# Performance work log

Measured on AMD Instinct MI355X. Metric: run time of the kernel, lower is better.

The kernel has to match this reference:

```python
import jax, jax.numpy as jnp
import numpy as np

B = 8192
D_IN = 1024
H = 1024
N_LAYERS = 10  # 1 input layer + 9 hidden layers, then output layer H->1


def setup_inputs() -> dict:
    key = jax.random.key(0)
    ks = jax.random.split(key, 7)
    s_in = 1.0 / np.sqrt(D_IN)
    s_h = 1.0 / np.sqrt(H)
    return {
        "x": jax.random.normal(ks[0], (B, D_IN), dtype=jnp.float32),
        "W0": jax.random.normal(ks[1], (H, D_IN), dtype=jnp.float32) * s_in,
        "b0": jax.random.normal(ks[2], (H,), dtype=jnp.float32) * s_in,
        "Wh": jax.random.normal(ks[3], (N_LAYERS - 1, H, H), dtype=jnp.float32) * s_h,
        "bh": jax.random.normal(ks[4], (N_LAYERS - 1, H), dtype=jnp.float32) * s_h,
        "Wout": jax.random.normal(ks[5], (1, H), dtype=jnp.float32) * s_h,
        "bout": jax.random.normal(ks[6], (1,), dtype=jnp.float32) * s_h,
    }


def reference(x, W0, b0, Wh, bh, Wout, bout):
    # First layer: Linear(D_IN -> H) + sigmoid. torch Linear is x @ W.T + b.
    h = jax.nn.sigmoid(x @ W0.T + b0)  # [B, H]

    # Remaining num_layers-1 hidden layers, identical shape -> lax.scan over stacked weights.
    def step(h, wb):
        W, b = wb
        return jax.nn.sigmoid(h @ W.T + b), None

    h, _ = jax.lax.scan(step, h, (Wh, bh))

    # Output layer: Linear(H -> 1), no activation.
    return h @ Wout.T + bout  # [B, 1]
```

## Files before the change

### kernel.cpp

```cpp
#include <hip/hip_runtime.h>
#include <stdint.h>

typedef unsigned short u16;
typedef unsigned int   u32;
typedef _Float16 f16;
typedef __attribute__((ext_vector_type(4))) float    f32x4;
typedef __attribute__((ext_vector_type(8))) _Float16 f16x8;
typedef __attribute__((ext_vector_type(4))) _Float16 f16x4;

#define DIM    1024
#define NROWS  8192
#define NLAYER 10

__device__ __forceinline__ void gl_lds16(const void* g, void* l) {
    __builtin_amdgcn_global_load_lds((const __attribute__((address_space(1))) u32*)g,
                                     (__attribute__((address_space(3))) u32*)l, 16, 0, 0);
}

__global__ __launch_bounds__(256) void conv_weights(const float* __restrict__ W0,
                                                    const float* __restrict__ Wh,
                                                    f16* __restrict__ Wf) {
    int i = (blockIdx.x * 256 + threadIdx.x) * 4;
    const float* src = (i < 1048576) ? (W0 + i) : (Wh + (i - 1048576));
    float4 w = *(const float4*)src;
    f16x4 o;
    o.x = (f16)w.x; o.y = (f16)w.y; o.z = (f16)w.z; o.w = (f16)w.w;
    *(f16x4*)(Wf + i) = o;
}

__global__ __launch_bounds__(256) void conv_x(const float* __restrict__ x,
                                              f16* __restrict__ Af) {
    int i = (blockIdx.x * 256 + threadIdx.x) * 4;
    float4 w = *(const float4*)(x + i);
    f16x4 o;
    o.x = (f16)w.x; o.y = (f16)w.y; o.z = (f16)w.z; o.w = (f16)w.w;
    *(f16x4*)(Af + i) = o;
}

#define ABUF_B 0
#define BBUF_B 16384
#define BUFSZ  32768
#define NKT    16

__global__ __launch_bounds__(256, 2) void layer_gemm(
        const f16* __restrict__ A,
        const f16* __restrict__ Bg,
        const float* __restrict__ bias,
        f16* __restrict__ O) {
    __shared__ char lds[2 * BUFSZ];

    int bid = blockIdx.x;
    int swz = (bid & 7) * 64 + (bid >> 3);
    int bn = swz & 7;
    int bm = swz >> 3;

    const int tid  = threadIdx.x;
    const int lane = tid & 63;
    const int wid  = tid >> 6;
    const int wr   = wid >> 1;
    const int wc   = wid & 1;

    const int swcol = (((lane & 7) ^ ((lane >> 3) & 7)) << 4);
    const char* gsrc[8];
    u32 ldst[8];
    #pragma unroll
    for (int j = 0; j < 8; ++j) {
        int c = wid * 8 + j;
        if (c < 16) {
            int grow = bm * 128 + c * 8 + (lane >> 3);
            gsrc[j] = (const char*)A + (size_t)grow * 2048 + swcol;
            ldst[j] = ABUF_B + c * 1024;
        } else {
            int c2 = c - 16;
            int grow = bn * 128 + c2 * 8 + (lane >> 3);
            gsrc[j] = (const char*)Bg + (size_t)grow * 2048 + swcol;
            ldst[j] = BBUF_B + c2 * 1024;
        }
    }

    f32x4 acc[4][4];
    #pragma unroll
    for (int mf = 0; mf < 4; ++mf)
        #pragma unroll
        for (int nf = 0; nf < 4; ++nf)
            acc[mf][nf] = (f32x4){0.f, 0.f, 0.f, 0.f};

    #pragma unroll
    for (int j = 0; j < 8; ++j)
        gl_lds16(gsrc[j], lds + ldst[j]);
    __syncthreads();

    for (int kt = 0; kt < NKT; ++kt) {
        const char* base = lds + (kt & 1) * BUFSZ;
        if (kt < NKT - 1) {
            char* nb = lds + ((kt + 1) & 1) * BUFSZ;
            #pragma unroll
            for (int j = 0; j < 8; ++j)
                gl_lds16(gsrc[j] + (size_t)(kt + 1) * 128, nb + ldst[j]);
        }

        #pragma unroll
        for (int ks = 0; ks < 2; ++ks) {
            f16x8 a[4], b[4];
            const int cb = ks * 64 + ((lane >> 4) << 4);
            #pragma unroll
            for (int mf = 0; mf < 4; ++mf) {
                int r = wr * 64 + mf * 16 + (lane & 15);
                int byt = r * 128 + (cb ^ ((r & 7) << 4));
                a[mf] = *(const f16x8*)(base + ABUF_B + byt);
            }
            #pragma unroll
            for (int nf = 0; nf < 4; ++nf) {
                int r = wc * 64 + nf * 16 + (lane & 15);
                int byt = r * 128 + (cb ^ ((r & 7) << 4));
                b[nf] = *(const f16x8*)(base + BBUF_B + byt);
            }
            __builtin_amdgcn_s_setprio(1);
            #pragma unroll
            for (int mf = 0; mf < 4; ++mf)
                #pragma unroll
                for (int nf = 0; nf < 4; ++nf)
                    acc[mf][nf] = __builtin_amdgcn_mfma_f32_16x16x32_f16(b[nf], a[mf], acc[mf][nf], 0, 0, 0);
            __builtin_amdgcn_s_setprio(0);
        }
        __syncthreads();
    }

    #pragma unroll
    for (int nf = 0; nf < 4; ++nf) {
        int gn0 = bn * 128 + wc * 64 + nf * 16 + ((lane >> 4) << 2);
        f32x4 b4 = *(const f32x4*)(bias + gn0);
        #pragma unroll
        for (int mf = 0; mf < 4; ++mf) {
            int gm = bm * 128 + wr * 64 + mf * 16 + (lane & 15);
            f16x4 o;
            #pragma unroll
            for (int j = 0; j < 4; ++j) {
                float z = acc[mf][nf][j] + b4[j];
                o[j] = (f16)(1.0f / (1.0f + __expf(-z)));
            }
            *(f16x4*)(O + (size_t)gm * DIM + gn0) = o;
        }
    }
}

__global__ __launch_bounds__(256) void out_gemv(const f16* __restrict__ A,
                                                const float* __restrict__ Wout,
                                                const float* __restrict__ bout,
                                                float* __restrict__ out) {
    int wid  = threadIdx.x >> 6;
    int lane = threadIdx.x & 63;
    int row  = blockIdx.x * 4 + wid;
    const f16* p = A + (size_t)row * DIM + lane * 16;
    const float* pw = Wout + lane * 16;
    float s = 0.f;
    #pragma unroll
    for (int i = 0; i < 4; ++i) {
        f16x4 h4 = *(const f16x4*)(p + i * 4);
        float4 w4 = *(const float4*)(pw + i * 4);
        s += (float)h4.x * w4.x + (float)h4.y * w4.y + (float)h4.z * w4.z + (float)h4.w * w4.w;
    }
    #pragma unroll
    for (int off = 32; off > 0; off >>= 1)
        s += __shfl_down(s, off);
    if (lane == 0) out[row] = s + bout[0];
}

extern "C" void kernel_launch(void* const* d_in, const int* in_sizes, int n_in,
                              void* d_out, int out_size, void* d_ws, size_t ws_size,
                              hipStream_t stream) {
    const float* x    = (const float*)d_in[0];
    const float* W0   = (const float*)d_in[1];
    const float* b0   = (const float*)d_in[2];
    const float* Wh   = (const float*)d_in[3];
    const float* bh   = (const float*)d_in[4];
    const float* Wout = (const float*)d_in[5];
    const float* bout = (const float*)d_in[6];
    float* out = (float*)d_out;

    f16* ws = (f16*)d_ws;
    f16* Wf = ws;
    f16* A0 = Wf + (size_t)NLAYER * DIM * DIM;
    f16* A1 = A0 + (size_t)NROWS * DIM;

    conv_weights<<<NLAYER * DIM * DIM / 1024, 256, 0, stream>>>(W0, Wh, Wf);
    conv_x<<<NROWS * DIM / 1024, 256, 0, stream>>>(x, A0);

    const f16* in = A0;
    f16* o = A1;
    for (int l = 0; l < NLAYER; ++l) {
        const float* bias = (l == 0) ? b0 : (bh + (size_t)(l - 1) * DIM);
        layer_gemm<<<512, 256, 0, stream>>>(in, Wf + (size_t)l * DIM * DIM, bias, o);
        f16* t = (f16*)in; in = o; o = t;
    }

    out_gemv<<<NROWS / 4, 256, 0, stream>>>(in, Wout, bout, out);
}
```

Baseline: 269.0 us.

## Prepack weights into MFMA fragment layout and load B directly to registers

Weights are converted into a fragment-packed layout so each lane can load its MFMA B operand straight from global memory into registers, bypassing LDS. The GEMM tile grows to 256x128 with 512 threads, and only the A tile is staged through double-buffered LDS, which cuts LDS traffic and reuses each B fragment across more rows. The cost is B loads going directly from global/L2 with latency exposed inside the k-loop, plus only 256 blocks on the device.

```diff
diff --git a/kernel.cpp b/kernel.cpp
--- a/kernel.cpp
+++ b/kernel.cpp
@@ -17,15 +17,26 @@
                                      (__attribute__((address_space(3))) u32*)l, 16, 0, 0);
 }
 
+__device__ __forceinline__ f16 cvt16(float x) { return (f16)x; }
+
 __global__ __launch_bounds__(256) void conv_weights(const float* __restrict__ W0,
                                                     const float* __restrict__ Wh,
-                                                    f16* __restrict__ Wf) {
-    int i = (blockIdx.x * 256 + threadIdx.x) * 4;
-    const float* src = (i < 1048576) ? (W0 + i) : (Wh + (i - 1048576));
-    float4 w = *(const float4*)src;
-    f16x4 o;
-    o.x = (f16)w.x; o.y = (f16)w.y; o.z = (f16)w.z; o.w = (f16)w.w;
-    *(f16x4*)(Wf + i) = o;
+                                                    f16* __restrict__ Wp) {
+    int g    = blockIdx.x * 4 + (threadIdx.x >> 6);
+    int lane = threadIdx.x & 63;
+    int lz   = g >> 11;
+    int rem  = g & 2047;
+    int n16  = rem >> 5;
+    int kc   = rem & 31;
+    int n  = n16 * 16 + (lane & 15);
+    int k0 = kc * 32 + (lane >> 4) * 8;
+    const float* src = (lz == 0 ? W0 : Wh + (size_t)(lz - 1) * DIM * DIM) + (size_t)n * DIM + k0;
+    float4 w0 = *(const float4*)src;
+    float4 w1 = *(const float4*)(src + 4);
+    f16x8 o;
+    o[0]=cvt16(w0.x); o[1]=cvt16(w0.y); o[2]=cvt16(w0.z); o[3]=cvt16(w0.w);
+    o[4]=cvt16(w1.x); o[5]=cvt16(w1.y); o[6]=cvt16(w1.z); o[7]=cvt16(w1.w);
+    *(f16x8*)((char*)Wp + (size_t)g * 1024 + lane * 16) = o;
 }
 
 __global__ __launch_bounds__(256) void conv_x(const float* __restrict__ x,
@@ -37,20 +48,18 @@
     *(f16x4*)(Af + i) = o;
 }
 
-#define ABUF_B 0
-#define BBUF_B 16384
-#define BUFSZ  32768
-#define NKT    16
-
-__global__ __launch_bounds__(256, 2) void layer_gemm(
+#define ABUF  32768
+#define NKT   16
+
+__global__ __launch_bounds__(512, 2) void layer_gemm(
         const f16* __restrict__ A,
-        const f16* __restrict__ Bg,
+        const f16* __restrict__ Bp,
         const float* __restrict__ bias,
         f16* __restrict__ O) {
-    __shared__ char lds[2 * BUFSZ];
+    __shared__ char lds[2 * ABUF];
 
     int bid = blockIdx.x;
-    int swz = (bid & 7) * 64 + (bid >> 3);
+    int swz = (bid & 7) * 32 + (bid >> 3);
     int bn = swz & 7;
     int bm = swz >> 3;
 
@@ -61,22 +70,18 @@
     const int wc   = wid & 1;
 
     const int swcol = (((lane & 7) ^ ((lane >> 3) & 7)) << 4);
-    const char* gsrc[8];
-    u32 ldst[8];
-    #pragma unroll
-    for (int j = 0; j < 8; ++j) {
-        int c = wid * 8 + j;
-        if (c < 16) {
-            int grow = bm * 128 + c * 8 + (lane >> 3);
-            gsrc[j] = (const char*)A + (size_t)grow * 2048 + swcol;
-            ldst[j] = ABUF_B + c * 1024;
-        } else {
-            int c2 = c - 16;
-            int grow = bn * 128 + c2 * 8 + (lane >> 3);
-            gsrc[j] = (const char*)Bg + (size_t)grow * 2048 + swcol;
-            ldst[j] = BBUF_B + c2 * 1024;
-        }
-    }
+    const char* gsrc[4];
+    u32 ldst[4];
+    #pragma unroll
+    for (int j = 0; j < 4; ++j) {
+        int c = wid * 4 + j;
+        int grow = bm * 256 + c * 8 + (lane >> 3);
+        gsrc[j] = (const char*)A + (size_t)grow * 2048 + swcol;
+        ldst[j] = c * 1024;
+    }
+
+    const char* bptr = (const char*)Bp
+                     + ((size_t)(bn * 8 + wc * 4) * 32) * 1024 + lane * 16;
 
     f32x4 acc[4][4];
     #pragma unroll
@@ -86,41 +91,42 @@
             acc[mf][nf] = (f32x4){0.f, 0.f, 0.f, 0.f};
 
     #pragma unroll
-    for (int j = 0; j < 8; ++j)
+    for (int j = 0; j < 4; ++j)
         gl_lds16(gsrc[j], lds + ldst[j]);
     __syncthreads();
 
     for (int kt = 0; kt < NKT; ++kt) {
-        const char* base = lds + (kt & 1) * BUFSZ;
+        f16x8 b[2][4];
+        #pragma unroll
+        for (int ks = 0; ks < 2; ++ks)
+            #pragma unroll
+            for (int nf = 0; nf < 4; ++nf)
+                b[ks][nf] = *(const f16x8*)(bptr + ((size_t)(nf * 32 + kt * 2 + ks)) * 1024);
+
         if (kt < NKT - 1) {
-            char* nb = lds + ((kt + 1) & 1) * BUFSZ;
-            #pragma unroll
-            for (int j = 0; j < 8; ++j)
+            char* nb = lds + ((kt + 1) & 1) * ABUF;
+            #pragma unroll
+            for (int j = 0; j < 4; ++j)
                 gl_lds16(gsrc[j] + (size_t)(kt + 1) * 128, nb + ldst[j]);
         }
 
+        const char* base = lds + (kt & 1) * ABUF;
         #pragma unroll
         for (int ks = 0; ks < 2; ++ks) {
-            f16x8 a[4], b[4];
+            f16x8 a[4];
             const int cb = ks * 64 + ((lane >> 4) << 4);
             #pragma unroll
             for (int mf = 0; mf < 4; ++mf) {
                 int r = wr * 64 + mf * 16 + (lane & 15);
                 int byt = r * 128 + (cb ^ ((r & 7) << 4));
-                a[mf] = *(const f16x8*)(base + ABUF_B + byt);
-            }
-            #pragma unroll
-            for (int nf = 0; nf < 4; ++nf) {
-                int r = wc * 64 + nf * 16 + (lane & 15);
-                int byt = r * 128 + (cb ^ ((r & 7) << 4));
-                b[nf] = *(const f16x8*)(base + BBUF_B + byt);
+                a[mf] = *(const f16x8*)(base + byt);
             }
             __builtin_amdgcn_s_setprio(1);
             #pragma unroll
             for (int mf = 0; mf < 4; ++mf)
                 #pragma unroll
                 for (int nf = 0; nf < 4; ++nf)
-                    acc[mf][nf] = __builtin_amdgcn_mfma_f32_16x16x32_f16(b[nf], a[mf], acc[mf][nf], 0, 0, 0);
+                    acc[mf][nf] = __builtin_amdgcn_mfma_f32_16x16x32_f16(b[ks][nf], a[mf], acc[mf][nf], 0, 0, 0);
             __builtin_amdgcn_s_setprio(0);
         }
         __syncthreads();
@@ -132,7 +138,7 @@
         f32x4 b4 = *(const f32x4*)(bias + gn0);
         #pragma unroll
         for (int mf = 0; mf < 4; ++mf) {
-            int gm = bm * 128 + wr * 64 + mf * 16 + (lane & 15);
+            int gm = bm * 256 + wr * 64 + mf * 16 + (lane & 15);
             f16x4 o;
             #pragma unroll
             for (int j = 0; j < 4; ++j) {
@@ -179,18 +185,18 @@
     float* out = (float*)d_out;
 
     f16* ws = (f16*)d_ws;
-    f16* Wf = ws;
-    f16* A0 = Wf + (size_t)NLAYER * DIM * DIM;
+    f16* Wp = ws;
+    f16* A0 = Wp + (size_t)NLAYER * DIM * DIM;
     f16* A1 = A0 + (size_t)NROWS * DIM;
 
-    conv_weights<<<NLAYER * DIM * DIM / 1024, 256, 0, stream>>>(W0, Wh, Wf);
+    conv_weights<<<NLAYER * 2048 / 4, 256, 0, stream>>>(W0, Wh, Wp);
     conv_x<<<NROWS * DIM / 1024, 256, 0, stream>>>(x, A0);
 
     const f16* in = A0;
     f16* o = A1;
     for (int l = 0; l < NLAYER; ++l) {
         const float* bias = (l == 0) ? b0 : (bh + (size_t)(l - 1) * DIM);
-        layer_gemm<<<512, 256, 0, stream>>>(in, Wf + (size_t)l * DIM * DIM, bias, o);
+        layer_gemm<<<256, 512, 0, stream>>>(in, Wp + (size_t)l * DIM * DIM, bias, o);
         f16* t = (f16*)in; in = o; o = t;
     }
 
```

Result: slower. 316.8 us (+17.8%).

## Single-buffer LDS in layer GEMM for higher occupancy and fuse conversion kernels

Applied to the files above, without the earlier changes.

Removes the double-buffered LDS prefetch in the layer GEMM, using one 32KB tile buffer loaded then synchronized each k-step, and raises the launch-bounds occupancy hint to 4 blocks per CU. Also merges the weight and input fp32->fp16 conversion kernels into a single launch. The intent is to rely on more resident blocks rather than software prefetch for latency hiding, but the grid of 512 blocks may not fill the extra slots, exposing load latency and tightening register limits.

```diff
diff --git a/kernel.cpp b/kernel.cpp
--- a/kernel.cpp
+++ b/kernel.cpp
@@ -17,37 +17,40 @@
                                      (__attribute__((address_space(3))) u32*)l, 16, 0, 0);
 }
 
-__global__ __launch_bounds__(256) void conv_weights(const float* __restrict__ W0,
-                                                    const float* __restrict__ Wh,
-                                                    f16* __restrict__ Wf) {
-    int i = (blockIdx.x * 256 + threadIdx.x) * 4;
-    const float* src = (i < 1048576) ? (W0 + i) : (Wh + (i - 1048576));
+#define WELEMS (NLAYER * DIM * DIM)
+#define XELEMS (NROWS * DIM)
+__global__ __launch_bounds__(256) void conv_all(const float* __restrict__ x,
+                                                const float* __restrict__ W0,
+                                                const float* __restrict__ Wh,
+                                                f16* __restrict__ Wf,
+                                                f16* __restrict__ A0) {
+    size_t i = ((size_t)blockIdx.x * 256 + threadIdx.x) * 4;
+    const float* src;
+    f16* dst;
+    if (i < WELEMS) {
+        src = (i < DIM * DIM) ? (W0 + i) : (Wh + (i - DIM * DIM));
+        dst = Wf + i;
+    } else {
+        size_t k = i - WELEMS;
+        src = x + k;
+        dst = A0 + k;
+    }
     float4 w = *(const float4*)src;
     f16x4 o;
     o.x = (f16)w.x; o.y = (f16)w.y; o.z = (f16)w.z; o.w = (f16)w.w;
-    *(f16x4*)(Wf + i) = o;
-}
-
-__global__ __launch_bounds__(256) void conv_x(const float* __restrict__ x,
-                                              f16* __restrict__ Af) {
-    int i = (blockIdx.x * 256 + threadIdx.x) * 4;
-    float4 w = *(const float4*)(x + i);
-    f16x4 o;
-    o.x = (f16)w.x; o.y = (f16)w.y; o.z = (f16)w.z; o.w = (f16)w.w;
-    *(f16x4*)(Af + i) = o;
+    *(f16x4*)dst = o;
 }
 
 #define ABUF_B 0
 #define BBUF_B 16384
-#define BUFSZ  32768
 #define NKT    16
 
-__global__ __launch_bounds__(256, 2) void layer_gemm(
+__global__ __launch_bounds__(256, 4) void layer_gemm(
         const f16* __restrict__ A,
         const f16* __restrict__ Bg,
         const float* __restrict__ bias,
         f16* __restrict__ O) {
-    __shared__ char lds[2 * BUFSZ];
+    __shared__ char lds[32768];
 
     int bid = blockIdx.x;
     int swz = (bid & 7) * 64 + (bid >> 3);
@@ -85,19 +88,11 @@
         for (int nf = 0; nf < 4; ++nf)
             acc[mf][nf] = (f32x4){0.f, 0.f, 0.f, 0.f};
 
-    #pragma unroll
-    for (int j = 0; j < 8; ++j)
-        gl_lds16(gsrc[j], lds + ldst[j]);
-    __syncthreads();
-
     for (int kt = 0; kt < NKT; ++kt) {
-        const char* base = lds + (kt & 1) * BUFSZ;
-        if (kt < NKT - 1) {
-            char* nb = lds + ((kt + 1) & 1) * BUFSZ;
-            #pragma unroll
-            for (int j = 0; j < 8; ++j)
-                gl_lds16(gsrc[j] + (size_t)(kt + 1) * 128, nb + ldst[j]);
-        }
+        #pragma unroll
+        for (int j = 0; j < 8; ++j)
+            gl_lds16(gsrc[j] + (size_t)kt * 128, lds + ldst[j]);
+        __syncthreads();
 
         #pragma unroll
         for (int ks = 0; ks < 2; ++ks) {
@@ -107,13 +102,13 @@
             for (int mf = 0; mf < 4; ++mf) {
                 int r = wr * 64 + mf * 16 + (lane & 15);
                 int byt = r * 128 + (cb ^ ((r & 7) << 4));
-                a[mf] = *(const f16x8*)(base + ABUF_B + byt);
+                a[mf] = *(const f16x8*)(lds + ABUF_B + byt);
             }
             #pragma unroll
             for (int nf = 0; nf < 4; ++nf) {
                 int r = wc * 64 + nf * 16 + (lane & 15);
                 int byt = r * 128 + (cb ^ ((r & 7) << 4));
-                b[nf] = *(const f16x8*)(base + BBUF_B + byt);
+                b[nf] = *(const f16x8*)(lds + BBUF_B + byt);
             }
             __builtin_amdgcn_s_setprio(1);
             #pragma unroll
@@ -180,11 +175,10 @@
 
     f16* ws = (f16*)d_ws;
     f16* Wf = ws;
-    f16* A0 = Wf + (size_t)NLAYER * DIM * DIM;
-    f16* A1 = A0 + (size_t)NROWS * DIM;
+    f16* A0 = Wf + (size_t)WELEMS;
+    f16* A1 = A0 + (size_t)XELEMS;
 
-    conv_weights<<<NLAYER * DIM * DIM / 1024, 256, 0, stream>>>(W0, Wh, Wf);
-    conv_x<<<NROWS * DIM / 1024, 256, 0, stream>>>(x, A0);
+    conv_all<<<(WELEMS + XELEMS) / 1024, 256, 0, stream>>>(x, W0, Wh, Wf, A0);
 
     const f16* in = A0;
     f16* o = A1;
```

Measured after the change: 267.7 us. Within noise of the previous version (-0.5%).
